# Kernel optimization log

Measured on AMD Instinct MI355X. Metric: run time of the kernel, lower is better.

The kernel has to match this reference:

```python
import jax, jax.numpy as jnp
import numpy as np

N_NODES = 100000
N_EDGES = 3200000
INPUT_DIM = 128
HIDDEN = 64


def spmm(row, col, vals, x, n):
    # out[i] = sum_{e: row[e]==i} vals[e] * x[col[e]]  -- COO SpMM via gather + segment_sum
    msgs = vals[:, None] * x[col]  # [E, F]
    return jax.ops.segment_sum(msgs, row, num_segments=n)


def setup_inputs() -> dict:
    key = jax.random.key(0)
    ks = jax.random.split(key, 12)
    embeddings = jax.random.normal(ks[0], (N_NODES, INPUT_DIM), dtype=jnp.float32)
    norm_degrees = jax.random.uniform(ks[1], (N_NODES, 1), dtype=jnp.float32)
    seed_mask = (jax.random.uniform(ks[2], (N_NODES, 1)) < 0.05).astype(jnp.float32)
    adj_row = jax.random.randint(ks[3], (N_EDGES,), 0, N_NODES, dtype=jnp.int32)
    adj_col = jax.random.randint(ks[4], (N_EDGES,), 0, N_NODES, dtype=jnp.int32)
    adj_vals = jax.random.uniform(ks[5], (N_EDGES,), dtype=jnp.float32)
    d_in = INPUT_DIM + 2
    # Linear params (torch Linear: y = x @ W.T + b); store W as [in, out]
    W1 = jax.random.normal(ks[6], (d_in, HIDDEN), dtype=jnp.float32) / np.sqrt(d_in)
    b1 = jnp.zeros((HIDDEN,), dtype=jnp.float32)
    W2 = jax.random.normal(ks[7], (HIDDEN, HIDDEN), dtype=jnp.float32) / np.sqrt(HIDDEN)
    b2 = jnp.zeros((HIDDEN,), dtype=jnp.float32)
    W_out = jax.random.normal(ks[8], (HIDDEN, 1), dtype=jnp.float32) / np.sqrt(HIDDEN)
    b_out = jnp.zeros((1,), dtype=jnp.float32)
    return {
        "embeddings": embeddings, "norm_degrees": norm_degrees, "seed_mask": seed_mask,
        "adj_row": adj_row, "adj_col": adj_col, "adj_vals": adj_vals,
        "W1": W1, "b1": b1, "W2": W2, "b2": b2, "W_out": W_out, "b_out": b_out,
    }


def reference(embeddings, norm_degrees, seed_mask, adj_row, adj_col, adj_vals,
              W1, b1, W2, b2, W_out, b_out):
    n = embeddings.shape[0]
    x = jnp.concatenate([embeddings, norm_degrees, seed_mask], axis=1)  # [N, input_dim+2]
    x = x @ W1 + b1                       # conv1
    x = jax.nn.relu(spmm(adj_row, adj_col, adj_vals, x, n))
    x = x @ W2 + b2                       # conv2
    x = jax.nn.relu(spmm(adj_row, adj_col, adj_vals, x, n))
    graph_rep = jnp.sum(x, axis=0)        # [HIDDEN]
    return graph_rep @ W_out + b_out      # [1]
```

## Files before the change

kernel.cpp:

```cpp
#include <hip/hip_runtime.h>
#include <hip/hip_bf16.h>

#define HID 64
#define IN_EMB 128
#define IN_DIM 130
#define ROWS_PER_BKT 512
#define LOG_RPB 9
#define MAX_BKT 256
#define PART_CHUNK 4096
#define SLOT_E 18432
#define W1TS 160
#define SASTR 168
#define SYSTR 72
#define RPB 32
#define ECAP 2048

typedef __hip_bfloat16 bf16;
typedef __attribute__((ext_vector_type(8))) short bf16x8;
typedef __attribute__((ext_vector_type(4))) float fx4;
typedef __attribute__((ext_vector_type(2))) float fx2;

__device__ __forceinline__ short f2bfs(float f) {
  __hip_bfloat16 h = __float2bfloat16(f);
  return *(reinterpret_cast<short*>(&h));
}
__device__ __forceinline__ int pk_fp8x4(float a, float b, float c, float d) {
  int v = __builtin_amdgcn_cvt_pk_fp8_f32(a, b, 0, false);
  v = __builtin_amdgcn_cvt_pk_fp8_f32(c, d, v, true);
  return v;
}
__device__ __forceinline__ unsigned char f2fp8(float x) {
  return (unsigned char)(__builtin_amdgcn_cvt_pk_fp8_f32(x, x, 0, false) & 0xFF);
}

__global__ __launch_bounds__(256) void wprep_kernel(
    const float* __restrict__ W1, const float* __restrict__ W2,
    short* __restrict__ w1t, short* __restrict__ w2t, int* __restrict__ bcur) {
  const int t = threadIdx.x;
  if (blockIdx.x == 0) {
    for (int idx = t; idx < 64 * W1TS; idx += 256) {
      int c = idx / W1TS, k = idx % W1TS;
      w1t[idx] = f2bfs((k < IN_DIM) ? W1[k * HID + c] : 0.f);
    }
  } else if (blockIdx.x == 1) {
    for (int idx = t; idx < 64 * 64; idx += 256) {
      int c = idx >> 6, k = idx & 63;
      w2t[idx] = f2bfs(W2[k * HID + c]);
    }
  } else {
    if (t < MAX_BKT) bcur[t] = 0;
  }
}

__global__ __launch_bounds__(512) void partition_kernel(
    const int* __restrict__ row, const int* __restrict__ col,
    const float* __restrict__ vals, int* __restrict__ bcur,
    int2* __restrict__ tmp, int nE) {
  __shared__ int2 lbuf[PART_CHUNK];
  __shared__ unsigned char lbid[PART_CHUNK];
  __shared__ int h[MAX_BKT];
  __shared__ int sc[MAX_BKT];
  __shared__ int lofs[MAX_BKT + 1];
  __shared__ int lcur[MAX_BKT];
  __shared__ int gbase[MAX_BKT];
  const int t = threadIdx.x;
  const int base = blockIdx.x * PART_CHUNK;
  const int cntE = min(PART_CHUNK, nE - base);

  if (t < MAX_BKT) h[t] = 0;
  __syncthreads();
  for (int kk = t; kk < PART_CHUNK / 4; kk += 512) {
    int e0 = base + kk * 4;
    if (e0 + 3 < nE) {
      int4 r4 = ((const int4*)row)[(base >> 2) + kk];
      atomicAdd(&h[r4.x >> LOG_RPB], 1);
      atomicAdd(&h[r4.y >> LOG_RPB], 1);
      atomicAdd(&h[r4.z >> LOG_RPB], 1);
      atomicAdd(&h[r4.w >> LOG_RPB], 1);
    } else {
      for (int j = 0; j < 4; ++j) {
        int e = e0 + j;
        if (e < nE) atomicAdd(&h[row[e] >> LOG_RPB], 1);
      }
    }
  }
  __syncthreads();
  if (t < MAX_BKT) sc[t] = h[t];
  __syncthreads();
  for (int off = 1; off < MAX_BKT; off <<= 1) {
    int u = (t < MAX_BKT && t >= off) ? sc[t - off] : 0;
    __syncthreads();
    if (t < MAX_BKT) sc[t] += u;
    __syncthreads();
  }
  if (t < MAX_BKT) {
    int ex = sc[t] - h[t];
    lofs[t] = ex;
    lcur[t] = ex;
    if (h[t] > 0) gbase[t] = t * SLOT_E + atomicAdd(&bcur[t], h[t]);
  }
  if (t == MAX_BKT - 1) lofs[MAX_BKT] = sc[t];
  __syncthreads();
  for (int kk = t; kk < PART_CHUNK / 4; kk += 512) {
    int e0 = base + kk * 4;
    if (e0 + 3 < nE) {
      int4 r4 = ((const int4*)row)[(base >> 2) + kk];
      int4 c4 = ((const int4*)col)[(base >> 2) + kk];
      float4 v4 = ((const float4*)vals)[(base >> 2) + kk];
      int rr[4] = {r4.x, r4.y, r4.z, r4.w};
      int cc[4] = {c4.x, c4.y, c4.z, c4.w};
      float vv[4] = {v4.x, v4.y, v4.z, v4.w};
#pragma unroll
      for (int j = 0; j < 4; ++j) {
        int b = rr[j] >> LOG_RPB;
        int p = atomicAdd(&lcur[b], 1);
        lbuf[p] = make_int2(cc[j] | ((rr[j] & (ROWS_PER_BKT - 1)) << 20),
                            __float_as_int(vv[j]));
        lbid[p] = (unsigned char)b;
      }
    } else {
      for (int j = 0; j < 4; ++j) {
        int e = e0 + j;
        if (e < nE) {
          int r = row[e];
          int b = r >> LOG_RPB;
          int p = atomicAdd(&lcur[b], 1);
          lbuf[p] = make_int2(col[e] | ((r & (ROWS_PER_BKT - 1)) << 20),
                              __float_as_int(vals[e]));
          lbid[p] = (unsigned char)b;
        }
      }
    }
  }
  __syncthreads();
  for (int i = t; i < cntE; i += 512) {
    int b = lbid[i];
    int off = i - lofs[b];
    int g = gbase[b] + off;
    if (g - b * SLOT_E < SLOT_E) tmp[g] = lbuf[i];
  }
}

__global__ __launch_bounds__(512) void bucket_sort_kernel(
    const int* __restrict__ bcurf, const int2* __restrict__ tmp,
    int2* __restrict__ ce, int* __restrict__ row_ptr, int n) {
  __shared__ int binc[MAX_BKT];
  __shared__ int bcnt_s[MAX_BKT];
  __shared__ int rcnt[ROWS_PER_BKT];
  __shared__ int rpos[ROWS_PER_BKT];
  __shared__ int sc[ROWS_PER_BKT];
  const int t = threadIdx.x;
  const int b = blockIdx.x;
  if (t < MAX_BKT) { int c = bcurf[t]; bcnt_s[t] = c; binc[t] = c; }
  __syncthreads();
  for (int off = 1; off < MAX_BKT; off <<= 1) {
    int u = (t < MAX_BKT && t >= off) ? binc[t - off] : 0;
    __syncthreads();
    if (t < MAX_BKT) binc[t] += u;
    __syncthreads();
  }
  const int start = binc[b] - bcnt_s[b];
  const int len   = bcnt_s[b];
  if (b == gridDim.x - 1 && t == 0) row_ptr[n] = binc[MAX_BKT - 1];
  const int2* ts = tmp + (size_t)b * SLOT_E;
  rcnt[t] = 0;
  __syncthreads();
  const int* keys = (const int*)ts;
  for (int i = t; i < len; i += 512)
    atomicAdd(&rcnt[((unsigned)keys[2 * i]) >> 20], 1);
  __syncthreads();
  sc[t] = rcnt[t];
  __syncthreads();
  for (int off = 1; off < ROWS_PER_BKT; off <<= 1) {
    int u = (t >= off) ? sc[t - off] : 0;
    __syncthreads();
    sc[t] += u;
    __syncthreads();
  }
  {
    int ex = sc[t] - rcnt[t];
    int gpos = start + ex;
    rpos[t] = gpos;
    int gr = b * ROWS_PER_BKT + t;
    if (gr < n) row_ptr[gr] = gpos;
  }
  __syncthreads();
  for (int i = t; i < len; i += 512) {
    int2 e = ts[i];
    int p = atomicAdd(&rpos[((unsigned)e.x) >> 20], 1);
    ce[p] = make_int2(e.x & 0xFFFFF, e.y);
  }
}

__global__ __launch_bounds__(256) void lin1_kernel(
    const float* __restrict__ emb, const float* __restrict__ deg,
    const float* __restrict__ seed, const short* __restrict__ w1t,
    const float* __restrict__ b1, unsigned char* __restrict__ out, int n) {
  __shared__ short sA[64 * SASTR];
  const int t = threadIdx.x;
  const int base = blockIdx.x * 64;

  for (int idx = t; idx < 64 * 32; idx += 256) {
    int nn = idx >> 5, k4 = idx & 31;
    int node = base + nn;
    short4 wv;
    if (node < n) {
      float4 v = ((const float4*)emb)[(size_t)node * 32 + k4];
      wv = make_short4(f2bfs(v.x), f2bfs(v.y), f2bfs(v.z), f2bfs(v.w));
    } else {
      wv = make_short4(0, 0, 0, 0);
    }
    *(short4*)&sA[nn * SASTR + 4 * k4] = wv;
  }
  for (int idx = t; idx < 64 * 32; idx += 256) {
    int nn = idx >> 5, kk = idx & 31;
    int node = base + nn;
    float v = 0.f;
    if (node < n) {
      if (kk == 0) v = deg[node];
      else if (kk == 1) v = seed[node];
    }
    sA[nn * SASTR + 128 + kk] = f2bfs(v);
  }
  __syncthreads();

  const int lane = t & 63, w = t >> 6;
  const int nl = lane & 15, q = lane >> 4;
  const short* pA = &sA[(w * 16 + nl) * SASTR + q * 8];
  const short* pB = w1t + nl * W1TS + q * 8;
  const float bias0 = b1[nl], bias1 = b1[16 + nl],
              bias2 = b1[32 + nl], bias3 = b1[48 + nl];

  fx4 ac0 = {0.f, 0.f, 0.f, 0.f}, ac1 = ac0, ac2 = ac0, ac3 = ac0;
#pragma unroll
  for (int kt = 0; kt < 5; ++kt) {
    bf16x8 a   = *(const bf16x8*)(pA + kt * 32);
    bf16x8 b0  = *(const bf16x8*)(pB + kt * 32);
    bf16x8 b1v = *(const bf16x8*)(pB + 16 * W1TS + kt * 32);
    bf16x8 b2v = *(const bf16x8*)(pB + 32 * W1TS + kt * 32);
    bf16x8 b3v = *(const bf16x8*)(pB + 48 * W1TS + kt * 32);
    ac0 = __builtin_amdgcn_mfma_f32_16x16x32_bf16(a, b0,  ac0, 0, 0, 0);
    ac1 = __builtin_amdgcn_mfma_f32_16x16x32_bf16(a, b1v, ac1, 0, 0, 0);
    ac2 = __builtin_amdgcn_mfma_f32_16x16x32_bf16(a, b2v, ac2, 0, 0, 0);
    ac3 = __builtin_amdgcn_mfma_f32_16x16x32_bf16(a, b3v, ac3, 0, 0, 0);
  }
#pragma unroll
  for (int r = 0; r < 4; ++r) {
    int node = base + w * 16 + q * 4 + r;
    if (node < n) {
      unsigned char* o = out + ((size_t)node << 6);
      o[nl]      = f2fp8(ac0[r] + bias0);
      o[16 + nl] = f2fp8(ac1[r] + bias1);
      o[32 + nl] = f2fp8(ac2[r] + bias2);
      o[48 + nl] = f2fp8(ac3[r] + bias3);
    }
  }
}

#define GLD(ev, u)                                                            \
  const uint2 u = *(const uint2*)(xp + (((size_t)(unsigned)(ev)) << 6) + 8 * fl);
#define GMAD(ev, u)                                                           \
  {                                                                           \
    const float v = __int_as_float((int)((ev) >> 32));                        \
    const fx2 v2 = {v, v};                                                    \
    a0 += v2 * __builtin_amdgcn_cvt_pk_f32_fp8(u.x, false);                   \
    a1 += v2 * __builtin_amdgcn_cvt_pk_f32_fp8(u.x, true);                    \
    a2 += v2 * __builtin_amdgcn_cvt_pk_f32_fp8(u.y, false);                   \
    a3 += v2 * __builtin_amdgcn_cvt_pk_f32_fp8(u.y, true);                    \
  }
#define GMAD_P(ev, u, ok)                                                     \
  {                                                                           \
    const float v = (ok) ? __int_as_float((int)((ev) >> 32)) : 0.f;           \
    const fx2 v2 = {v, v};                                                    \
    a0 += v2 * __builtin_amdgcn_cvt_pk_f32_fp8(u.x, false);                   \
    a1 += v2 * __builtin_amdgcn_cvt_pk_f32_fp8(u.x, true);                    \
    a2 += v2 * __builtin_amdgcn_cvt_pk_f32_fp8(u.y, false);                   \
    a3 += v2 * __builtin_amdgcn_cvt_pk_f32_fp8(u.y, true);                    \
  }

#define SPMM_STAGE_EDGES                                                      \
  const unsigned long long* cep = (const unsigned long long*)ce;              \
  const int r0blk = blockIdx.x * RPB;                                         \
  const int bstartE = row_ptr[r0blk];                                         \
  const int bendE = row_ptr[(r0blk + RPB < n) ? (r0blk + RPB) : n];           \
  const int cnt = min(bendE - bstartE, ECAP);                                 \
  for (int ii = threadIdx.x; ii < cnt; ii += 256)                             \
    eb[ii] = __builtin_nontemporal_load(cep + bstartE + ii);                  \
  __syncthreads();

#define SPMM_GATHER_BODY                                                      \
  const int i0r = row_ptr[r];                                                 \
  const int endr = row_ptr[r + 1];                                            \
  const int lend = endr - bstartE;                                            \
  if (lend <= cnt) {                                                          \
    int i = i0r - bstartE;                                                    \
    for (; i + 4 <= lend; i += 4) {                                           \
      unsigned long long e0 = eb[i];                                          \
      unsigned long long e1 = eb[i + 1];                                      \
      unsigned long long e2 = eb[i + 2];                                      \
      unsigned long long e3 = eb[i + 3];                                      \
      GLD(e0, u0); GLD(e1, u1); GLD(e2, u2); GLD(e3, u3);                     \
      GMAD(e0, u0); GMAD(e1, u1); GMAD(e2, u2); GMAD(e3, u3);                 \
    }                                                                         \
    if (i < lend) {                                                           \
      const int last = lend - 1;                                              \
      bool k1 = i + 1 < lend, k2 = i + 2 < lend, k3 = i + 3 < lend;           \
      unsigned long long e0 = eb[i];                                          \
      unsigned long long e1 = eb[k1 ? i + 1 : last];                          \
      unsigned long long e2 = eb[k2 ? i + 2 : last];                          \
      unsigned long long e3 = eb[k3 ? i + 3 : last];                          \
      GLD(e0, u0); GLD(e1, u1); GLD(e2, u2); GLD(e3, u3);                     \
      GMAD(e0, u0); GMAD_P(e1, u1, k1);                                       \
      GMAD_P(e2, u2, k2); GMAD_P(e3, u3, k3);                                 \
    }                                                                         \
  } else {                                                                    \
    int i = i0r;                                                              \
    for (; i + 4 <= endr; i += 4) {                                           \
      unsigned long long e0 = __builtin_nontemporal_load(cep + i);            \
      unsigned long long e1 = __builtin_nontemporal_load(cep + i + 1);        \
      unsigned long long e2 = __builtin_nontemporal_load(cep + i + 2);        \
      unsigned long long e3 = __builtin_nontemporal_load(cep + i + 3);        \
      GLD(e0, u0); GLD(e1, u1); GLD(e2, u2); GLD(e3, u3);                     \
      GMAD(e0, u0); GMAD(e1, u1); GMAD(e2, u2); GMAD(e3, u3);                 \
    }                                                                         \
    if (i < endr) {                                                           \
      const int last = endr - 1;                                              \
      bool k1 = i + 1 < endr, k2 = i + 2 < endr, k3 = i + 3 < endr;           \
      unsigned long long e0 = cep[i];                                         \
      unsigned long long e1 = cep[k1 ? i + 1 : last];                         \
      unsigned long long e2 = cep[k2 ? i + 2 : last];                         \
      unsigned long long e3 = cep[k3 ? i + 3 : last];                         \
      GLD(e0, u0); GLD(e1, u1); GLD(e2, u2); GLD(e3, u3);                     \
      GMAD(e0, u0); GMAD_P(e1, u1, k1);                                       \
      GMAD_P(e2, u2, k2); GMAD_P(e3, u3, k3);                                 \
    }                                                                         \
  }

__global__ __launch_bounds__(256) void spmm1_lin2_kernel(
    const int* __restrict__ row_ptr, const int2* __restrict__ ce,
    const unsigned char* __restrict__ x, const short* __restrict__ w2t,
    const float* __restrict__ b2, unsigned char* __restrict__ xout, int n) {
  __shared__ unsigned long long eb[ECAP];
  __shared__ unsigned char sY[RPB * SYSTR];
  const int fl = threadIdx.x & 7;
  const int sg = threadIdx.x >> 3;
  const int r = blockIdx.x * RPB + sg;
  const unsigned char* xp = x;
  SPMM_STAGE_EDGES
  int lo = 0, hi = 0;
  if (r < n) {
    fx2 a0 = {0.f, 0.f}, a1 = a0, a2 = a0, a3 = a0;
    SPMM_GATHER_BODY
    lo = pk_fp8x4(fmaxf(a0.x, 0.f), fmaxf(a0.y, 0.f),
                  fmaxf(a1.x, 0.f), fmaxf(a1.y, 0.f));
    hi = pk_fp8x4(fmaxf(a2.x, 0.f), fmaxf(a2.y, 0.f),
                  fmaxf(a3.x, 0.f), fmaxf(a3.y, 0.f));
  }
  *(int2*)&sY[sg * SYSTR + 8 * fl] = make_int2(lo, hi);
  __syncthreads();

  const int lane = threadIdx.x & 63, w = threadIdx.x >> 6;
  const int nl = lane & 15, q = lane >> 4;
  const int rowg = (w & 1) * 16;
  const int colg = (w >> 1) * 32;
  const unsigned char* pY = &sY[(rowg + nl) * SYSTR + q * 8];
  const short* pB = w2t + (colg + nl) * 64 + q * 8;
  const float bias0 = b2[colg + nl], bias1 = b2[colg + 16 + nl];
  fx4 ac0 = {0.f, 0.f, 0.f, 0.f}, ac1 = ac0;
#pragma unroll
  for (int kt = 0; kt < 2; ++kt) {
    uint2 u8 = *(const uint2*)(pY + kt * 32);
    fx2 f0 = __builtin_amdgcn_cvt_pk_f32_fp8(u8.x, false);
    fx2 f1 = __builtin_amdgcn_cvt_pk_f32_fp8(u8.x, true);
    fx2 f2 = __builtin_amdgcn_cvt_pk_f32_fp8(u8.y, false);
    fx2 f3 = __builtin_amdgcn_cvt_pk_f32_fp8(u8.y, true);
    bf16x8 a;
    a[0] = f2bfs(f0.x); a[1] = f2bfs(f0.y); a[2] = f2bfs(f1.x); a[3] = f2bfs(f1.y);
    a[4] = f2bfs(f2.x); a[5] = f2bfs(f2.y); a[6] = f2bfs(f3.x); a[7] = f2bfs(f3.y);
    bf16x8 b0  = *(const bf16x8*)(pB + kt * 32);
    bf16x8 b1v = *(const bf16x8*)(pB + 16 * 64 + kt * 32);
    ac0 = __builtin_amdgcn_mfma_f32_16x16x32_bf16(a, b0,  ac0, 0, 0, 0);
    ac1 = __builtin_amdgcn_mfma_f32_16x16x32_bf16(a, b1v, ac1, 0, 0, 0);
  }
#pragma unroll
  for (int r2 = 0; r2 < 4; ++r2) {
    int node = blockIdx.x * RPB + rowg + q * 4 + r2;
    if (node < n) {
      unsigned char* o = xout + ((size_t)node << 6);
      o[colg + nl]      = f2fp8(ac0[r2] + bias0);
      o[colg + 16 + nl] = f2fp8(ac1[r2] + bias1);
    }
  }
}

__global__ __launch_bounds__(256) void spmm2_fused_kernel(
    const int* __restrict__ row_ptr, const int2* __restrict__ ce,
    const unsigned char* __restrict__ x, const float* __restrict__ Wout,
    float* __restrict__ partials, int n) {
  __shared__ unsigned long long eb[ECAP];
  const int fl = threadIdx.x & 7;
  const int r = blockIdx.x * RPB + (threadIdx.x >> 3);
  const unsigned char* xp = x;
  SPMM_STAGE_EDGES
  float wpart = 0.f;
  if (r < n) {
    fx2 a0 = {0.f, 0.f}, a1 = a0, a2 = a0, a3 = a0;
    SPMM_GATHER_BODY
    const float4 wv0 = ((const float4*)Wout)[2 * fl];
    const float4 wv1 = ((const float4*)Wout)[2 * fl + 1];
    wpart = fmaxf(a0.x, 0.f) * wv0.x + fmaxf(a0.y, 0.f) * wv0.y
          + fmaxf(a1.x, 0.f) * wv0.z + fmaxf(a1.y, 0.f) * wv0.w
          + fmaxf(a2.x, 0.f) * wv1.x + fmaxf(a2.y, 0.f) * wv1.y
          + fmaxf(a3.x, 0.f) * wv1.z + fmaxf(a3.y, 0.f) * wv1.w;
  }
  for (int off = 32; off; off >>= 1) wpart += __shfl_down(wpart, off, 64);
  __shared__ float part[4];
  const int lane = threadIdx.x & 63;
  if (lane == 0) part[threadIdx.x >> 6] = wpart;
  __syncthreads();
  if (threadIdx.x == 0)
    partials[blockIdx.x] = part[0] + part[1] + part[2] + part[3];
}

__global__ __launch_bounds__(1024) void reduce_kernel(
    const float* __restrict__ partials, const float* __restrict__ bout,
    float* __restrict__ out, int m) {
  const int t = threadIdx.x;
  float s = 0.f;
  const int m4 = m >> 2;
  for (int i = t; i < m4; i += 1024) {
    float4 v = ((const float4*)partials)[i];
    s += v.x + v.y + v.z + v.w;
  }
  if (t < (m & 3)) s += partials[(m & ~3) + t];
  for (int off = 32; off; off >>= 1) s += __shfl_down(s, off, 64);
  __shared__ float wsum[16];
  if ((t & 63) == 0) wsum[t >> 6] = s;
  __syncthreads();
  if (t == 0) {
    float tot = bout[0];
    for (int w = 0; w < 16; ++w) tot += wsum[w];
    out[0] = tot;
  }
}

extern "C" void kernel_launch(void* const* d_in, const int* in_sizes, int n_in,
                              void* d_out, int out_size, void* d_ws, size_t ws_size,
                              hipStream_t stream) {
  const float* emb  = (const float*)d_in[0];
  const float* deg  = (const float*)d_in[1];
  const float* seed = (const float*)d_in[2];
  const int*   row  = (const int*)d_in[3];
  const int*   col  = (const int*)d_in[4];
  const float* vals = (const float*)d_in[5];
  const float* W1   = (const float*)d_in[6];
  const float* b1   = (const float*)d_in[7];
  const float* W2   = (const float*)d_in[8];
  const float* b2   = (const float*)d_in[9];
  const float* Wout = (const float*)d_in[10];
  const float* bout = (const float*)d_in[11];
  float* out = (float*)d_out;

  const int n  = in_sizes[0] / IN_EMB;
  const int nE = in_sizes[3];
  const int nbkt = (n + ROWS_PER_BKT - 1) / ROWS_PER_BKT;

  const int lin_blocks  = (n + 63) / 64;
  const int row_blocks  = (n + RPB - 1) / RPB;
  const int part_blocks = (nE + PART_CHUNK - 1) / PART_CHUNK;

  char* ws = (char*)d_ws;
  int2* ce   = (int2*)ws;  ws += (size_t)nE * sizeof(int2);
  char* tmpb = ws;
  int2* tmp  = (int2*)ws;  ws += (size_t)nbkt * SLOT_E * sizeof(int2);
  unsigned char* xb = (unsigned char*)ws;  ws += ((size_t)n * HID + 255) & ~255ULL;
  int* row_ptr = (int*)ws; ws += ((size_t)(n + 1) * 4 + 255) & ~255ULL;
  int* bcur    = (int*)ws; ws += ((size_t)MAX_BKT * 4 + 255) & ~255ULL;
  short* w1t   = (short*)ws; ws += ((size_t)64 * W1TS * 2 + 255) & ~255ULL;
  short* w2t   = (short*)ws; ws += ((size_t)64 * 64 * 2 + 255) & ~255ULL;
  float* partials = (float*)ws;
  unsigned char* xa = (unsigned char*)tmpb;

  wprep_kernel<<<3, 256, 0, stream>>>(W1, W2, w1t, w2t, bcur);
  partition_kernel<<<part_blocks, 512, 0, stream>>>(row, col, vals, bcur, tmp, nE);
  bucket_sort_kernel<<<nbkt, 512, 0, stream>>>(bcur, tmp, ce, row_ptr, n);

  lin1_kernel<<<lin_blocks, 256, 0, stream>>>(emb, deg, seed, w1t, b1, xa, n);
  spmm1_lin2_kernel<<<row_blocks, 256, 0, stream>>>(row_ptr, ce, xa, w2t, b2, xb, n);
  spmm2_fused_kernel<<<row_blocks, 256, 0, stream>>>(row_ptr, ce, xb, Wout, partials, n);
  reduce_kernel<<<1, 1024, 0, stream>>>(partials, bout, out, row_blocks);
}
```

Measured before the change: 286.3 us.

## Merge edge partition and lin1 GEMM into one heterogeneous kernel launch

Combines the COO edge partition kernel and the first linear layer into a single launch. Block index decides the role: the first blocks partition edges, the rest run the lin1 MFMA on 128 nodes per 512-thread block. The two phases can now overlap on the GPU and one launch is saved. Because they run concurrently, lin1 output no longer reuses the tmp partition buffer and gets its own workspace region, which costs extra memory.

```diff
diff --git a/kernel.cpp b/kernel.cpp
--- a/kernel.cpp
+++ b/kernel.cpp
@@ -14,6 +14,8 @@
 #define SYSTR 72
 #define RPB 32
 #define ECAP 2048
+#define LIN1_NPB 128
+#define SMEM_BYTES 43008
 
 typedef __hip_bfloat16 bf16;
 typedef __attribute__((ext_vector_type(8))) short bf16x8;
@@ -52,92 +54,159 @@
   }
 }
 
-__global__ __launch_bounds__(512) void partition_kernel(
+__global__ __launch_bounds__(512) void build_lin1_kernel(
     const int* __restrict__ row, const int* __restrict__ col,
     const float* __restrict__ vals, int* __restrict__ bcur,
-    int2* __restrict__ tmp, int nE) {
-  __shared__ int2 lbuf[PART_CHUNK];
-  __shared__ unsigned char lbid[PART_CHUNK];
-  __shared__ int h[MAX_BKT];
-  __shared__ int sc[MAX_BKT];
-  __shared__ int lofs[MAX_BKT + 1];
-  __shared__ int lcur[MAX_BKT];
-  __shared__ int gbase[MAX_BKT];
+    int2* __restrict__ tmp, int nE,
+    const float* __restrict__ emb, const float* __restrict__ deg,
+    const float* __restrict__ seed, const short* __restrict__ w1t,
+    const float* __restrict__ b1, unsigned char* __restrict__ xa,
+    int n, int part_blocks) {
+  __shared__ __align__(16) char smem[SMEM_BYTES];
   const int t = threadIdx.x;
-  const int base = blockIdx.x * PART_CHUNK;
-  const int cntE = min(PART_CHUNK, nE - base);
-
-  if (t < MAX_BKT) h[t] = 0;
-  __syncthreads();
-  for (int kk = t; kk < PART_CHUNK / 4; kk += 512) {
-    int e0 = base + kk * 4;
-    if (e0 + 3 < nE) {
-      int4 r4 = ((const int4*)row)[(base >> 2) + kk];
-      atomicAdd(&h[r4.x >> LOG_RPB], 1);
-      atomicAdd(&h[r4.y >> LOG_RPB], 1);
-      atomicAdd(&h[r4.z >> LOG_RPB], 1);
-      atomicAdd(&h[r4.w >> LOG_RPB], 1);
-    } else {
-      for (int j = 0; j < 4; ++j) {
-        int e = e0 + j;
-        if (e < nE) atomicAdd(&h[row[e] >> LOG_RPB], 1);
+
+  if ((int)blockIdx.x < part_blocks) {
+    int2* lbuf = (int2*)smem;
+    unsigned char* lbid = (unsigned char*)(smem + 32768);
+    int* h     = (int*)(smem + 36864);
+    int* sc    = (int*)(smem + 37888);
+    int* lofs  = (int*)(smem + 38912);
+    int* lcur  = (int*)(smem + 39952);
+    int* gbase = (int*)(smem + 40976);
+    const int base = blockIdx.x * PART_CHUNK;
+    const int cntE = min(PART_CHUNK, nE - base);
+
+    if (t < MAX_BKT) h[t] = 0;
+    __syncthreads();
+    for (int kk = t; kk < PART_CHUNK / 4; kk += 512) {
+      int e0 = base + kk * 4;
+      if (e0 + 3 < nE) {
+        int4 r4 = ((const int4*)row)[(base >> 2) + kk];
+        atomicAdd(&h[r4.x >> LOG_RPB], 1);
+        atomicAdd(&h[r4.y >> LOG_RPB], 1);
+        atomicAdd(&h[r4.z >> LOG_RPB], 1);
+        atomicAdd(&h[r4.w >> LOG_RPB], 1);
+      } else {
+        for (int j = 0; j < 4; ++j) {
+          int e = e0 + j;
+          if (e < nE) atomicAdd(&h[row[e] >> LOG_RPB], 1);
+        }
       }
     }
-  }
-  __syncthreads();
-  if (t < MAX_BKT) sc[t] = h[t];
-  __syncthreads();
-  for (int off = 1; off < MAX_BKT; off <<= 1) {
-    int u = (t < MAX_BKT && t >= off) ? sc[t - off] : 0;
-    __syncthreads();
-    if (t < MAX_BKT) sc[t] += u;
-    __syncthreads();
-  }
-  if (t < MAX_BKT) {
-    int ex = sc[t] - h[t];
-    lofs[t] = ex;
-    lcur[t] = ex;
-    if (h[t] > 0) gbase[t] = t * SLOT_E + atomicAdd(&bcur[t], h[t]);
-  }
-  if (t == MAX_BKT - 1) lofs[MAX_BKT] = sc[t];
-  __syncthreads();
-  for (int kk = t; kk < PART_CHUNK / 4; kk += 512) {
-    int e0 = base + kk * 4;
-    if (e0 + 3 < nE) {
-      int4 r4 = ((const int4*)row)[(base >> 2) + kk];
-      int4 c4 = ((const int4*)col)[(base >> 2) + kk];
-      float4 v4 = ((const float4*)vals)[(base >> 2) + kk];
-      int rr[4] = {r4.x, r4.y, r4.z, r4.w};
-      int cc[4] = {c4.x, c4.y, c4.z, c4.w};
-      float vv[4] = {v4.x, v4.y, v4.z, v4.w};
+    __syncthreads();
+    if (t < MAX_BKT) sc[t] = h[t];
+    __syncthreads();
+    for (int off = 1; off < MAX_BKT; off <<= 1) {
+      int u = (t < MAX_BKT && t >= off) ? sc[t - off] : 0;
+      __syncthreads();
+      if (t < MAX_BKT) sc[t] += u;
+      __syncthreads();
+    }
+    if (t < MAX_BKT) {
+      int ex = sc[t] - h[t];
+      lofs[t] = ex;
+      lcur[t] = ex;
+      if (h[t] > 0) gbase[t] = t * SLOT_E + atomicAdd(&bcur[t], h[t]);
+    }
+    if (t == MAX_BKT - 1) lofs[MAX_BKT] = sc[t];
+    __syncthreads();
+    for (int kk = t; kk < PART_CHUNK / 4; kk += 512) {
+      int e0 = base + kk * 4;
+      if (e0 + 3 < nE) {
+        int4 r4 = ((const int4*)row)[(base >> 2) + kk];
+        int4 c4 = ((const int4*)col)[(base >> 2) + kk];
+        float4 v4 = ((const float4*)vals)[(base >> 2) + kk];
+        int rr[4] = {r4.x, r4.y, r4.z, r4.w};
+        int cc[4] = {c4.x, c4.y, c4.z, c4.w};
+        float vv[4] = {v4.x, v4.y, v4.z, v4.w};
 #pragma unroll
-      for (int j = 0; j < 4; ++j) {
-        int b = rr[j] >> LOG_RPB;
-        int p = atomicAdd(&lcur[b], 1);
-        lbuf[p] = make_int2(cc[j] | ((rr[j] & (ROWS_PER_BKT - 1)) << 20),
-                            __float_as_int(vv[j]));
-        lbid[p] = (unsigned char)b;
-      }
-    } else {
-      for (int j = 0; j < 4; ++j) {
-        int e = e0 + j;
-        if (e < nE) {
-          int r = row[e];
-          int b = r >> LOG_RPB;
+        for (int j = 0; j < 4; ++j) {
+          int b = rr[j] >> LOG_RPB;
           int p = atomicAdd(&lcur[b], 1);
-          lbuf[p] = make_int2(col[e] | ((r & (ROWS_PER_BKT - 1)) << 20),
-                              __float_as_int(vals[e]));
+          lbuf[p] = make_int2(cc[j] | ((rr[j] & (ROWS_PER_BKT - 1)) << 20),
+                              __float_as_int(vv[j]));
           lbid[p] = (unsigned char)b;
         }
+      } else {
+        for (int j = 0; j < 4; ++j) {
+          int e = e0 + j;
+          if (e < nE) {
+            int r = row[e];
+            int b = r >> LOG_RPB;
+            int p = atomicAdd(&lcur[b], 1);
+            lbuf[p] = make_int2(col[e] | ((r & (ROWS_PER_BKT - 1)) << 20),
+                                __float_as_int(vals[e]));
+            lbid[p] = (unsigned char)b;
+          }
+        }
       }
     }
-  }
-  __syncthreads();
-  for (int i = t; i < cntE; i += 512) {
-    int b = lbid[i];
-    int off = i - lofs[b];
-    int g = gbase[b] + off;
-    if (g - b * SLOT_E < SLOT_E) tmp[g] = lbuf[i];
+    __syncthreads();
+    for (int i = t; i < cntE; i += 512) {
+      int b = lbid[i];
+      int off = i - lofs[b];
+      int g = gbase[b] + off;
+      if (g - b * SLOT_E < SLOT_E) tmp[g] = lbuf[i];
+    }
+  } else {
+    short* sA = (short*)smem;
+    const int base = (blockIdx.x - part_blocks) * LIN1_NPB;
+
+    for (int idx = t; idx < LIN1_NPB * 32; idx += 512) {
+      int nn = idx >> 5, k4 = idx & 31;
+      int node = base + nn;
+      short4 wv;
+      if (node < n) {
+        float4 v = ((const float4*)emb)[(size_t)node * 32 + k4];
+        wv = make_short4(f2bfs(v.x), f2bfs(v.y), f2bfs(v.z), f2bfs(v.w));
+      } else {
+        wv = make_short4(0, 0, 0, 0);
+      }
+      *(short4*)&sA[nn * SASTR + 4 * k4] = wv;
+    }
+    for (int idx = t; idx < LIN1_NPB * 32; idx += 512) {
+      int nn = idx >> 5, kk = idx & 31;
+      int node = base + nn;
+      float v = 0.f;
+      if (node < n) {
+        if (kk == 0) v = deg[node];
+        else if (kk == 1) v = seed[node];
+      }
+      sA[nn * SASTR + 128 + kk] = f2bfs(v);
+    }
+    __syncthreads();
+
+    const int lane = t & 63, w = t >> 6;
+    const int nl = lane & 15, q = lane >> 4;
+    const short* pA = &sA[(w * 16 + nl) * SASTR + q * 8];
+    const short* pB = w1t + nl * W1TS + q * 8;
+    const float bias0 = b1[nl], bias1 = b1[16 + nl],
+                bias2 = b1[32 + nl], bias3 = b1[48 + nl];
+
+    fx4 ac0 = {0.f, 0.f, 0.f, 0.f}, ac1 = ac0, ac2 = ac0, ac3 = ac0;
+#pragma unroll
+    for (int kt = 0; kt < 5; ++kt) {
+      bf16x8 a   = *(const bf16x8*)(pA + kt * 32);
+      bf16x8 b0  = *(const bf16x8*)(pB + kt * 32);
+      bf16x8 b1v = *(const bf16x8*)(pB + 16 * W1TS + kt * 32);
+      bf16x8 b2v = *(const bf16x8*)(pB + 32 * W1TS + kt * 32);
+      bf16x8 b3v = *(const bf16x8*)(pB + 48 * W1TS + kt * 32);
+      ac0 = __builtin_amdgcn_mfma_f32_16x16x32_bf16(a, b0,  ac0, 0, 0, 0);
+      ac1 = __builtin_amdgcn_mfma_f32_16x16x32_bf16(a, b1v, ac1, 0, 0, 0);
+      ac2 = __builtin_amdgcn_mfma_f32_16x16x32_bf16(a, b2v, ac2, 0, 0, 0);
+      ac3 = __builtin_amdgcn_mfma_f32_16x16x32_bf16(a, b3v, ac3, 0, 0, 0);
+    }
+#pragma unroll
+    for (int r = 0; r < 4; ++r) {
+      int node = base + w * 16 + q * 4 + r;
+      if (node < n) {
+        unsigned char* o = xa + ((size_t)node << 6);
+        o[nl]      = f2fp8(ac0[r] + bias0);
+        o[16 + nl] = f2fp8(ac1[r] + bias1);
+        o[32 + nl] = f2fp8(ac2[r] + bias2);
+        o[48 + nl] = f2fp8(ac3[r] + bias3);
+      }
+    }
   }
 }
 
@@ -189,71 +258,6 @@
     int2 e = ts[i];
     int p = atomicAdd(&rpos[((unsigned)e.x) >> 20], 1);
     ce[p] = make_int2(e.x & 0xFFFFF, e.y);
-  }
-}
-
-__global__ __launch_bounds__(256) void lin1_kernel(
-    const float* __restrict__ emb, const float* __restrict__ deg,
-    const float* __restrict__ seed, const short* __restrict__ w1t,
-    const float* __restrict__ b1, unsigned char* __restrict__ out, int n) {
-  __shared__ short sA[64 * SASTR];
-  const int t = threadIdx.x;
-  const int base = blockIdx.x * 64;
-
-  for (int idx = t; idx < 64 * 32; idx += 256) {
-    int nn = idx >> 5, k4 = idx & 31;
-    int node = base + nn;
-    short4 wv;
-    if (node < n) {
-      float4 v = ((const float4*)emb)[(size_t)node * 32 + k4];
-      wv = make_short4(f2bfs(v.x), f2bfs(v.y), f2bfs(v.z), f2bfs(v.w));
-    } else {
-      wv = make_short4(0, 0, 0, 0);
-    }
-    *(short4*)&sA[nn * SASTR + 4 * k4] = wv;
-  }
-  for (int idx = t; idx < 64 * 32; idx += 256) {
-    int nn = idx >> 5, kk = idx & 31;
-    int node = base + nn;
-    float v = 0.f;
-    if (node < n) {
-      if (kk == 0) v = deg[node];
-      else if (kk == 1) v = seed[node];
-    }
-    sA[nn * SASTR + 128 + kk] = f2bfs(v);
-  }
-  __syncthreads();
-
-  const int lane = t & 63, w = t >> 6;
-  const int nl = lane & 15, q = lane >> 4;
-  const short* pA = &sA[(w * 16 + nl) * SASTR + q * 8];
-  const short* pB = w1t + nl * W1TS + q * 8;
-  const float bias0 = b1[nl], bias1 = b1[16 + nl],
-              bias2 = b1[32 + nl], bias3 = b1[48 + nl];
-
-  fx4 ac0 = {0.f, 0.f, 0.f, 0.f}, ac1 = ac0, ac2 = ac0, ac3 = ac0;
-#pragma unroll
-  for (int kt = 0; kt < 5; ++kt) {
-    bf16x8 a   = *(const bf16x8*)(pA + kt * 32);
-    bf16x8 b0  = *(const bf16x8*)(pB + kt * 32);
-    bf16x8 b1v = *(const bf16x8*)(pB + 16 * W1TS + kt * 32);
-    bf16x8 b2v = *(const bf16x8*)(pB + 32 * W1TS + kt * 32);
-    bf16x8 b3v = *(const bf16x8*)(pB + 48 * W1TS + kt * 32);
-    ac0 = __builtin_amdgcn_mfma_f32_16x16x32_bf16(a, b0,  ac0, 0, 0, 0);
-    ac1 = __builtin_amdgcn_mfma_f32_16x16x32_bf16(a, b1v, ac1, 0, 0, 0);
-    ac2 = __builtin_amdgcn_mfma_f32_16x16x32_bf16(a, b2v, ac2, 0, 0, 0);
-    ac3 = __builtin_amdgcn_mfma_f32_16x16x32_bf16(a, b3v, ac3, 0, 0, 0);
-  }
-#pragma unroll
-  for (int r = 0; r < 4; ++r) {
-    int node = base + w * 16 + q * 4 + r;
-    if (node < n) {
-      unsigned char* o = out + ((size_t)node << 6);
-      o[nl]      = f2fp8(ac0[r] + bias0);
-      o[16 + nl] = f2fp8(ac1[r] + bias1);
-      o[32 + nl] = f2fp8(ac2[r] + bias2);
-      o[48 + nl] = f2fp8(ac3[r] + bias3);
-    }
   }
 }
 
@@ -465,7 +469,7 @@
   const int nE = in_sizes[3];
   const int nbkt = (n + ROWS_PER_BKT - 1) / ROWS_PER_BKT;
 
-  const int lin_blocks  = (n + 63) / 64;
+  const int lin1_blocks = (n + LIN1_NPB - 1) / LIN1_NPB;
   const int row_blocks  = (n + RPB - 1) / RPB;
   const int part_blocks = (nE + PART_CHUNK - 1) / PART_CHUNK;
 
@@ -473,19 +477,21 @@
   int2* ce   = (int2*)ws;  ws += (size_t)nE * sizeof(int2);
   char* tmpb = ws;
   int2* tmp  = (int2*)ws;  ws += (size_t)nbkt * SLOT_E * sizeof(int2);
+  unsigned char* xa = (unsigned char*)ws;  ws += ((size_t)n * HID + 255) & ~255ULL;
   unsigned char* xb = (unsigned char*)ws;  ws += ((size_t)n * HID + 255) & ~255ULL;
   int* row_ptr = (int*)ws; ws += ((size_t)(n + 1) * 4 + 255) & ~255ULL;
   int* bcur    = (int*)ws; ws += ((size_t)MAX_BKT * 4 + 255) & ~255ULL;
   short* w1t   = (short*)ws; ws += ((size_t)64 * W1TS * 2 + 255) & ~255ULL;
   short* w2t   = (short*)ws; ws += ((size_t)64 * 64 * 2 + 255) & ~255ULL;
   float* partials = (float*)ws;
-  unsigned char* xa = (unsigned char*)tmpb;
+  (void)tmpb;
 
   wprep_kernel<<<3, 256, 0, stream>>>(W1, W2, w1t, w2t, bcur);
-  partition_kernel<<<part_blocks, 512, 0, stream>>>(row, col, vals, bcur, tmp, nE);
+  build_lin1_kernel<<<part_blocks + lin1_blocks, 512, 0, stream>>>(
+      row, col, vals, bcur, tmp, nE,
+      emb, deg, seed, w1t, b1, xa, n, part_blocks);
   bucket_sort_kernel<<<nbkt, 512, 0, stream>>>(bcur, tmp, ce, row_ptr, n);
 
-  lin1_kernel<<<lin_blocks, 256, 0, stream>>>(emb, deg, seed, w1t, b1, xa, n);
   spmm1_lin2_kernel<<<row_blocks, 256, 0, stream>>>(row_ptr, ce, xa, w2t, b2, xb, n);
   spmm2_fused_kernel<<<row_blocks, 256, 0, stream>>>(row_ptr, ce, xb, Wout, partials, n);
   reduce_kernel<<<1, 1024, 0, stream>>>(partials, bout, out, row_blocks);
```

Result: no change. 283.1 us (-1.1%).
